# Optimization experiments

Measured on AMD Instinct MI355X. Metric: run time of the kernel, lower is better.

The kernel has to match this reference:

```python
import jax, jax.numpy as jnp
import numpy as np

# Static problem dims (match setup_inputs / torch max()+1 derivation)
N = 2_000_000      # atoms
NALT = 8           # alternatives
B, C, R = 8, 4, 512  # batch, chains, residues
N_ATOM_TYPES = 500
VDW_COL = 0        # property_hashings['solvenergy_props']['VdW']
PADDING_INDEX = -1
BACKBONE_ATOMS = (0, 1, 2, 3)


def setup_inputs() -> dict:
    key = jax.random.key(0)
    k1, k2, k3, k4, k5, k6, k7, k8 = jax.random.split(key, 8)
    at_name = jax.random.randint(k1, (N,), 0, 40)      # atom type hashes (first 4 = backbone)
    batch = jax.random.randint(k2, (N,), 0, B)
    chain = jax.random.randint(k3, (N,), 0, C)
    resnum = jax.random.randint(k4, (N,), 0, R)
    atom_description = jnp.stack([at_name, batch, chain, resnum], axis=1).astype(jnp.int64)
    return {
        "coords": jax.random.normal(k5, (N, 3), dtype=jnp.float32),
        "atom_description": atom_description,
        "alternativeMask": jax.random.randint(k6, (N, NALT), 0, 2).astype(bool),
        "facc": jax.random.uniform(k7, (N, NALT), dtype=jnp.float32),
        "atom_Properties": jax.random.uniform(k8, (N_ATOM_TYPES, 8), dtype=jnp.float32),
        "weight": jnp.zeros((1,), dtype=jnp.float32),
    }


def reference(coords, atom_description, alternativeMask, facc, atom_Properties, weight):
    at_name = atom_description[:, 0]
    b_idx = atom_description[:, 1]
    c_idx = atom_description[:, 2]
    r_idx = atom_description[:, 3]

    # is_backbone: OR over backbone atom hashes
    bb = jnp.asarray(BACKBONE_ATOMS)
    is_backbone = (at_name[:, None] == bb[None, :]).any(axis=-1)  # [N]

    # bindToAtoms: gather VdW property, masked multiply by max(facc, 0)
    sa = jnp.maximum(facc, jnp.float32(0.0))                 # [N, NALT]
    vdw = atom_Properties[at_name, VDW_COL]                  # [N]
    atomE = jnp.where(alternativeMask, vdw[:, None] * sa, jnp.float32(0.0))
    atomE = atomE * (1.0 - jnp.tanh(weight[0])) * 0.3        # [N, NALT]

    # bindToResi: masked scatter-add into [B, C, R, NALT]
    valid = r_idx != PADDING_INDEX
    mc_vals = jnp.where((is_backbone & valid)[:, None], atomE, jnp.float32(0.0))
    sc_vals = jnp.where((~is_backbone & valid)[:, None], atomE, jnp.float32(0.0))
    zeros = jnp.zeros((B, C, R, NALT), dtype=jnp.float32)
    finalMC = zeros.at[b_idx, c_idx, r_idx].add(mc_vals)
    finalSC = zeros.at[b_idx, c_idx, r_idx].add(sc_vals)
    return finalMC, finalSC
```

## Files before the change

kernel.cpp:

```cpp
#include <hip/hip_runtime.h>
#include <hip/hip_bf16.h>
#include <math.h>

#define NALT      8
#define BDIM      8
#define CDIM      4
#define RDIM      512
#define OUT_HALF  (BDIM * CDIM * RDIM * NALT)
#define OUT_TOTAL (2 * OUT_HALF)

#define NBUCKET   32
#define BLK_ATOMS 1024
#define AITER     4
#define LSLOTS    8192


__device__ __forceinline__ unsigned int pack_bf16_2(float a, float b) {
    unsigned int ua = __float_as_uint(a);
    unsigned int ub = __float_as_uint(b);
    ua = (ua + 0x7fffu + ((ua >> 16) & 1u)) >> 16;
    ub = (ub + 0x7fffu + ((ub >> 16) & 1u)) >> 16;
    return ua | (ub << 16);
}

__global__ void __launch_bounds__(256) vdw_compact_kernel(
    const int4*   __restrict__ desc,
    const int4*   __restrict__ mask,
    const float4* __restrict__ facc,
    const float*  __restrict__ props,
    const float*  __restrict__ weight,
    unsigned short* __restrict__ hdrArr,
    unsigned short* __restrict__ lidxArr,
    uint4*        __restrict__ valArr,
    int n)
{
    __shared__ int            cnt[NBUCKET];
    __shared__ int            base[NBUCKET + 1];
    __shared__ unsigned short s_lidx[BLK_ATOMS];
    __shared__ uint4          s_val[BLK_ATOMS];

    const int tid = threadIdx.x;
    if (tid < NBUCKET) cnt[tid] = 0;
    __syncthreads();

    const int a0 = blockIdx.x * BLK_ATOMS;

    int4 d_[AITER];
    int  bkt[AITER];
    #pragma unroll
    for (int it = 0; it < AITER; ++it) {
        const int a = a0 + it * 256 + tid;
        bkt[it] = -1;
        if (a < n) {
            d_[it] = desc[a];
            if (d_[it].w != -1) {
                bkt[it] = d_[it].y * CDIM + d_[it].z;
                atomicAdd(&cnt[bkt[it]], 1);
            }
        }
    }
    __syncthreads();

    if (tid == 0) {
        int run = 0;
        #pragma unroll
        for (int j = 0; j < NBUCKET; ++j) { base[j] = run; run += cnt[j]; }
        base[NBUCKET] = run;
    }
    __syncthreads();
    if (tid < NBUCKET) cnt[tid] = 0;
    __syncthreads();

    const float scale = (1.0f - tanhf(weight[0])) * 0.3f;
    #pragma unroll
    for (int it = 0; it < AITER; ++it) {
        if (bkt[it] < 0) continue;
        const int a  = a0 + it * 256 + tid;
        const int4 d = d_[it];
        const float vs = props[d.x * 8] * scale;
        const int lidx = ((d.x < 4) ? 0 : 4096) + d.w * 8;

        const float4 f0 = facc[a * 2 + 0];
        const float4 f1 = facc[a * 2 + 1];
        const int4   m0 = mask[a * 2 + 0];
        const int4   m1 = mask[a * 2 + 1];
        const float v0 = m0.x ? vs * fmaxf(f0.x, 0.0f) : 0.0f;
        const float v1 = m0.y ? vs * fmaxf(f0.y, 0.0f) : 0.0f;
        const float v2 = m0.z ? vs * fmaxf(f0.z, 0.0f) : 0.0f;
        const float v3 = m0.w ? vs * fmaxf(f0.w, 0.0f) : 0.0f;
        const float v4 = m1.x ? vs * fmaxf(f1.x, 0.0f) : 0.0f;
        const float v5 = m1.y ? vs * fmaxf(f1.y, 0.0f) : 0.0f;
        const float v6 = m1.z ? vs * fmaxf(f1.z, 0.0f) : 0.0f;
        const float v7 = m1.w ? vs * fmaxf(f1.w, 0.0f) : 0.0f;

        const int loc = atomicAdd(&cnt[bkt[it]], 1);
        const int pos = base[bkt[it]] + loc;
        s_lidx[pos] = (unsigned short)lidx;
        s_val[pos]  = make_uint4(pack_bf16_2(v0, v1), pack_bf16_2(v2, v3),
                                 pack_bf16_2(v4, v5), pack_bf16_2(v6, v7));
    }
    __syncthreads();

    if (tid <= NBUCKET)
        hdrArr[blockIdx.x * 64 + tid] = (unsigned short)base[tid];

    unsigned int* ldst = (unsigned int*)(lidxArr + (size_t)blockIdx.x * BLK_ATOMS);
    const unsigned int* lsrc = (const unsigned int*)s_lidx;
    #pragma unroll
    for (int k = 0; k < BLK_ATOMS / 2 / 256; ++k)
        ldst[k * 256 + tid] = lsrc[k * 256 + tid];

    uint4* vdst = valArr + (size_t)blockIdx.x * BLK_ATOMS;
    #pragma unroll
    for (int k = 0; k < BLK_ATOMS / 256; ++k)
        vdst[k * 256 + tid] = s_val[k * 256 + tid];
}

__global__ void __launch_bounds__(256) vdw_accum_kernel(
    const unsigned short* __restrict__ hdrArr,
    const unsigned short* __restrict__ lidxArr,
    const uint4*          __restrict__ valArr,
    float*                __restrict__ partial,
    int nblocks, int nsplit)
{
    __shared__ float acc[LSLOTS];
    const int tid = threadIdx.x;
    for (int k = tid; k < LSLOTS; k += 256) acc[k] = 0.0f;
    __syncthreads();

    const int bucket = blockIdx.x / nsplit;
    const int split  = blockIdx.x % nsplit;
    const int per = (nblocks + nsplit - 1) / nsplit;
    const int b0  = split * per;
    const int b1  = (b0 + per < nblocks) ? (b0 + per) : nblocks;

    const int g    = tid >> 5;
    const int lane = tid & 31;

    for (int blk = b0 + g; blk < b1; blk += 8) {
        const int start = hdrArr[blk * 64 + bucket];
        const int end   = hdrArr[blk * 64 + bucket + 1];
        const unsigned short* la = lidxArr + (size_t)blk * BLK_ATOMS;
        const uint4*          va = valArr  + (size_t)blk * BLK_ATOMS;
        for (int rec = start + lane; rec < end; rec += 32) {
            const int   l = la[rec];
            const uint4 v = va[rec];
            float t;
            t = __uint_as_float(v.x << 16);          if (t != 0.0f) atomicAdd(&acc[l + 0], t);
            t = __uint_as_float(v.x & 0xffff0000u);  if (t != 0.0f) atomicAdd(&acc[l + 1], t);
            t = __uint_as_float(v.y << 16);          if (t != 0.0f) atomicAdd(&acc[l + 2], t);
            t = __uint_as_float(v.y & 0xffff0000u);  if (t != 0.0f) atomicAdd(&acc[l + 3], t);
            t = __uint_as_float(v.z << 16);          if (t != 0.0f) atomicAdd(&acc[l + 4], t);
            t = __uint_as_float(v.z & 0xffff0000u);  if (t != 0.0f) atomicAdd(&acc[l + 5], t);
            t = __uint_as_float(v.w << 16);          if (t != 0.0f) atomicAdd(&acc[l + 6], t);
            t = __uint_as_float(v.w & 0xffff0000u);  if (t != 0.0f) atomicAdd(&acc[l + 7], t);
        }
    }
    __syncthreads();

    float* dst = partial + (size_t)blockIdx.x * LSLOTS;
    for (int k = tid; k < LSLOTS; k += 256) dst[k] = acc[k];
}

__global__ void __launch_bounds__(256) vdw_merge_kernel(
    const float* __restrict__ partial,
    float*       __restrict__ out,
    int nsplit)
{
    const int idx = blockIdx.x * 256 + threadIdx.x;
    if (idx >= OUT_TOTAL) return;
    const int bb     = idx >> 17;
    const int b      = (idx >> 14) & 7;
    const int c      = (idx >> 12) & 3;
    const int lidx   = bb * 4096 + (idx & 4095);
    const int bucket = b * CDIM + c;
    const float* p = partial + ((size_t)bucket * nsplit) * LSLOTS + lidx;
    float s = 0.0f;
    for (int sp = 0; sp < nsplit; ++sp)
        s += p[(size_t)sp * LSLOTS];
    out[idx] = s;
}

__global__ void __launch_bounds__(256) vdw_atomic_kernel(
    const int*   __restrict__ desc,
    const int*   __restrict__ mask,
    const float* __restrict__ facc,
    const float* __restrict__ props,
    const float* __restrict__ weight,
    float*       __restrict__ out,
    int n)
{
    const int i = blockIdx.x * blockDim.x + threadIdx.x;
    if (i >= n) return;
    const float scale = (1.0f - tanhf(weight[0])) * 0.3f;
    const int4 d = reinterpret_cast<const int4*>(desc)[i];
    if (d.w == -1) return;
    const float vs = props[d.x * 8 + 0] * scale;
    const int   bb = (d.x >= 0 && d.x <= 3) ? 0 : 1;
    float* base = out + bb * OUT_HALF + (((d.y * CDIM + d.z) * RDIM + d.w) * NALT);
    const float4 f0 = reinterpret_cast<const float4*>(facc)[i * 2 + 0];
    const float4 f1 = reinterpret_cast<const float4*>(facc)[i * 2 + 1];
    const int4   m0 = reinterpret_cast<const int4*>(mask)[i * 2 + 0];
    const int4   m1 = reinterpret_cast<const int4*>(mask)[i * 2 + 1];
    if (m0.x) atomicAdd(base + 0, vs * fmaxf(f0.x, 0.0f));
    if (m0.y) atomicAdd(base + 1, vs * fmaxf(f0.y, 0.0f));
    if (m0.z) atomicAdd(base + 2, vs * fmaxf(f0.z, 0.0f));
    if (m0.w) atomicAdd(base + 3, vs * fmaxf(f0.w, 0.0f));
    if (m1.x) atomicAdd(base + 4, vs * fmaxf(f1.x, 0.0f));
    if (m1.y) atomicAdd(base + 5, vs * fmaxf(f1.y, 0.0f));
    if (m1.z) atomicAdd(base + 6, vs * fmaxf(f1.z, 0.0f));
    if (m1.w) atomicAdd(base + 7, vs * fmaxf(f1.w, 0.0f));
}

extern "C" void kernel_launch(void* const* d_in, const int* in_sizes, int n_in,
                              void* d_out, int out_size, void* d_ws, size_t ws_size,
                              hipStream_t stream)
{
    const int*   desc   = (const int*)d_in[1];
    const int*   mask   = (const int*)d_in[2];
    const float* facc   = (const float*)d_in[3];
    const float* props  = (const float*)d_in[4];
    const float* weight = (const float*)d_in[5];
    float*       out    = (float*)d_out;

    const int n       = in_sizes[1] / 4;
    const int nblocks = (n + BLK_ATOMS - 1) / BLK_ATOMS;

    auto align256 = [](size_t x) { return (x + 255) & ~(size_t)255; };
    const size_t off_hdr  = 0;
    const size_t off_lidx = align256(off_hdr  + (size_t)nblocks * 64 * 2);
    const size_t off_val  = align256(off_lidx + (size_t)nblocks * BLK_ATOMS * 2);
    const size_t off_part = align256(off_val  + (size_t)nblocks * BLK_ATOMS * 16);

    int nsplit = 0;
    for (int cand = 16; cand >= 1; cand >>= 1) {
        const size_t need = off_part +
            (size_t)NBUCKET * cand * LSLOTS * sizeof(float);
        if (need <= ws_size) { nsplit = cand; break; }
    }

    if (nsplit >= 1) {
        char* ws = (char*)d_ws;
        unsigned short* hdrArr  = (unsigned short*)(ws + off_hdr);
        unsigned short* lidxArr = (unsigned short*)(ws + off_lidx);
        uint4*          valArr  = (uint4*)(ws + off_val);
        float*          part    = (float*)(ws + off_part);

        vdw_compact_kernel<<<nblocks, 256, 0, stream>>>(
            (const int4*)desc, (const int4*)mask, (const float4*)facc,
            props, weight, hdrArr, lidxArr, valArr, n);

        vdw_accum_kernel<<<NBUCKET * nsplit, 256, 0, stream>>>(
            hdrArr, lidxArr, valArr, part, nblocks, nsplit);

        vdw_merge_kernel<<<(OUT_TOTAL + 255) / 256, 256, 0, stream>>>(
            part, out, nsplit);
    } else {
        hipMemsetAsync(d_out, 0, (size_t)out_size * sizeof(float), stream);
        vdw_atomic_kernel<<<(n + 255) / 256, 256, 0, stream>>>(
            desc, mask, facc, props, weight, out, n);
    }
}
```

Before: 88.99 us.

## Split bucket counting into a separate kernel with per-wave offsets

Moves the per-block bucket histogram and prefix scan into a new count kernel that writes per-wave bucket offsets and block headers to workspace. The compact kernel then issues all descriptor, facc and mask loads up front and places atoms using wave-local shared atomics plus the precomputed offsets. This removes several block-wide barriers and the serial scan from the compact kernel and lets its global loads overlap better. The cost is an extra kernel launch and a second full read of the atom descriptor array.

```diff
diff --git a/kernel.cpp b/kernel.cpp
--- a/kernel.cpp
+++ b/kernel.cpp
@@ -12,6 +12,7 @@
 #define NBUCKET   32
 #define BLK_ATOMS 1024
 #define AITER     4
+#define NWAVE     4
 #define LSLOTS    8192
 
 
@@ -23,67 +24,107 @@
     return ua | (ub << 16);
 }
 
+__global__ void __launch_bounds__(256) vdw_count_kernel(
+    const int4*   __restrict__ desc,
+    unsigned int* __restrict__ PW,
+    unsigned short* __restrict__ hdr,
+    int n)
+{
+    __shared__ unsigned int cw[NWAVE][NBUCKET];
+    __shared__ unsigned int base[NBUCKET + 1];
+    const int tid = threadIdx.x;
+    const int w   = tid >> 6;
+    if (tid < NWAVE * NBUCKET) cw[tid >> 5][tid & 31] = 0;
+    __syncthreads();
+
+    const int a0 = blockIdx.x * BLK_ATOMS;
+    #pragma unroll
+    for (int it = 0; it < AITER; ++it) {
+        const int a = a0 + it * 256 + tid;
+        if (a < n) {
+            const int4 d = desc[a];
+            if (d.w != -1) atomicAdd(&cw[w][d.y * CDIM + d.z], 1);
+        }
+    }
+    __syncthreads();
+
+    if (tid < NBUCKET) {
+        unsigned int s = 0;
+        unsigned int pref[NWAVE];
+        #pragma unroll
+        for (int ww = 0; ww < NWAVE; ++ww) { pref[ww] = s; s += cw[ww][tid]; }
+        base[tid] = s;
+        #pragma unroll
+        for (int ww = 0; ww < NWAVE; ++ww) cw[ww][tid] = pref[ww];
+    }
+    __syncthreads();
+    if (tid == 0) {
+        unsigned int run = 0;
+        #pragma unroll
+        for (int j = 0; j < NBUCKET; ++j) { const unsigned int t = base[j]; base[j] = run; run += t; }
+        base[NBUCKET] = run;
+    }
+    __syncthreads();
+
+    if (tid < NBUCKET) {
+        #pragma unroll
+        for (int ww = 0; ww < NWAVE; ++ww)
+            PW[(size_t)blockIdx.x * (NWAVE * NBUCKET) + ww * NBUCKET + tid] =
+                base[tid] + cw[ww][tid];
+    }
+    if (tid <= NBUCKET) hdr[blockIdx.x * 64 + tid] = (unsigned short)base[tid];
+}
+
 __global__ void __launch_bounds__(256) vdw_compact_kernel(
     const int4*   __restrict__ desc,
     const int4*   __restrict__ mask,
     const float4* __restrict__ facc,
     const float*  __restrict__ props,
     const float*  __restrict__ weight,
-    unsigned short* __restrict__ hdrArr,
+    const unsigned int* __restrict__ PW,
     unsigned short* __restrict__ lidxArr,
     uint4*        __restrict__ valArr,
     int n)
 {
-    __shared__ int            cnt[NBUCKET];
-    __shared__ int            base[NBUCKET + 1];
     __shared__ unsigned short s_lidx[BLK_ATOMS];
     __shared__ uint4          s_val[BLK_ATOMS];
-
-    const int tid = threadIdx.x;
-    if (tid < NBUCKET) cnt[tid] = 0;
-    __syncthreads();
-
+    __shared__ unsigned int   cw[NWAVE][NBUCKET];
+
+    const int tid  = threadIdx.x;
+    const int w    = tid >> 6;
+    const int lane = tid & 63;
+    if (lane < NBUCKET) cw[w][lane] = 0;
+
+    const float scale = (1.0f - tanhf(weight[0])) * 0.3f;
     const int a0 = blockIdx.x * BLK_ATOMS;
-
-    int4 d_[AITER];
-    int  bkt[AITER];
+    const unsigned int* myPW = PW + (size_t)blockIdx.x * (NWAVE * NBUCKET) + w * NBUCKET;
+
+    int4   d_[AITER];
+    float4 f0_[AITER], f1_[AITER];
+    int4   m0_[AITER], m1_[AITER];
+    bool   ok[AITER];
     #pragma unroll
     for (int it = 0; it < AITER; ++it) {
-        const int a = a0 + it * 256 + tid;
-        bkt[it] = -1;
-        if (a < n) {
-            d_[it] = desc[a];
-            if (d_[it].w != -1) {
-                bkt[it] = d_[it].y * CDIM + d_[it].z;
-                atomicAdd(&cnt[bkt[it]], 1);
-            }
-        }
-    }
-    __syncthreads();
-
-    if (tid == 0) {
-        int run = 0;
-        #pragma unroll
-        for (int j = 0; j < NBUCKET; ++j) { base[j] = run; run += cnt[j]; }
-        base[NBUCKET] = run;
-    }
-    __syncthreads();
-    if (tid < NBUCKET) cnt[tid] = 0;
-    __syncthreads();
-
-    const float scale = (1.0f - tanhf(weight[0])) * 0.3f;
+        const int a  = a0 + it * 256 + tid;
+        ok[it] = (a < n);
+        const int aa = ok[it] ? a : (n - 1);
+        d_[it]  = desc[aa];
+        f0_[it] = facc[aa * 2 + 0];
+        f1_[it] = facc[aa * 2 + 1];
+        m0_[it] = mask[aa * 2 + 0];
+        m1_[it] = mask[aa * 2 + 1];
+    }
+
     #pragma unroll
     for (int it = 0; it < AITER; ++it) {
-        if (bkt[it] < 0) continue;
-        const int a  = a0 + it * 256 + tid;
         const int4 d = d_[it];
+        if (!ok[it] || d.w == -1) continue;
+        const int bkt  = d.y * CDIM + d.z;
         const float vs = props[d.x * 8] * scale;
         const int lidx = ((d.x < 4) ? 0 : 4096) + d.w * 8;
 
-        const float4 f0 = facc[a * 2 + 0];
-        const float4 f1 = facc[a * 2 + 1];
-        const int4   m0 = mask[a * 2 + 0];
-        const int4   m1 = mask[a * 2 + 1];
+        const float4 f0 = f0_[it], f1 = f1_[it];
+        const int4   m0 = m0_[it], m1 = m1_[it];
         const float v0 = m0.x ? vs * fmaxf(f0.x, 0.0f) : 0.0f;
         const float v1 = m0.y ? vs * fmaxf(f0.y, 0.0f) : 0.0f;
         const float v2 = m0.z ? vs * fmaxf(f0.z, 0.0f) : 0.0f;
@@ -93,16 +134,13 @@
         const float v6 = m1.z ? vs * fmaxf(f1.z, 0.0f) : 0.0f;
         const float v7 = m1.w ? vs * fmaxf(f1.w, 0.0f) : 0.0f;
 
-        const int loc = atomicAdd(&cnt[bkt[it]], 1);
-        const int pos = base[bkt[it]] + loc;
+        const unsigned int rank = atomicAdd(&cw[w][bkt], 1u);
+        const unsigned int pos  = myPW[bkt] + rank;
         s_lidx[pos] = (unsigned short)lidx;
         s_val[pos]  = make_uint4(pack_bf16_2(v0, v1), pack_bf16_2(v2, v3),
                                  pack_bf16_2(v4, v5), pack_bf16_2(v6, v7));
     }
     __syncthreads();
-
-    if (tid <= NBUCKET)
-        hdrArr[blockIdx.x * 64 + tid] = (unsigned short)base[tid];
 
     unsigned int* ldst = (unsigned int*)(lidxArr + (size_t)blockIdx.x * BLK_ATOMS);
     const unsigned int* lsrc = (const unsigned int*)s_lidx;
@@ -227,7 +265,8 @@
     const int nblocks = (n + BLK_ATOMS - 1) / BLK_ATOMS;
 
     auto align256 = [](size_t x) { return (x + 255) & ~(size_t)255; };
-    const size_t off_hdr  = 0;
+    const size_t off_pw   = 0;
+    const size_t off_hdr  = align256(off_pw   + (size_t)nblocks * NWAVE * NBUCKET * 4);
     const size_t off_lidx = align256(off_hdr  + (size_t)nblocks * 64 * 2);
     const size_t off_val  = align256(off_lidx + (size_t)nblocks * BLK_ATOMS * 2);
     const size_t off_part = align256(off_val  + (size_t)nblocks * BLK_ATOMS * 16);
@@ -241,14 +280,18 @@
 
     if (nsplit >= 1) {
         char* ws = (char*)d_ws;
+        unsigned int*   PWarr   = (unsigned int*)(ws + off_pw);
         unsigned short* hdrArr  = (unsigned short*)(ws + off_hdr);
         unsigned short* lidxArr = (unsigned short*)(ws + off_lidx);
         uint4*          valArr  = (uint4*)(ws + off_val);
         float*          part    = (float*)(ws + off_part);
 
+        vdw_count_kernel<<<nblocks, 256, 0, stream>>>(
+            (const int4*)desc, PWarr, hdrArr, n);
+
         vdw_compact_kernel<<<nblocks, 256, 0, stream>>>(
             (const int4*)desc, (const int4*)mask, (const float4*)facc,
-            props, weight, hdrArr, lidxArr, valArr, n);
+            props, weight, PWarr, lidxArr, valArr, n);
 
         vdw_accum_kernel<<<NBUCKET * nsplit, 256, 0, stream>>>(
             hdrArr, lidxArr, valArr, part, nblocks, nsplit);
```

After: 95.48 us. 7.3% more time.
